# Kernel tuning notes

Measured on AMD Instinct MI355X. Metric: run time of the kernel, lower is better.

Reference implementation:

```python
import jax, jax.numpy as jnp
import numpy as np


def setup_inputs() -> dict:
    key = jax.random.key(0)
    k1, k2, k3 = jax.random.split(key, 3)
    B, E, N, D = 32, 8192, 2048, 128
    messages = jax.random.normal(k1, (B, E, D), dtype=jnp.float32)
    tgt_indices = jax.random.randint(k2, (B, E), 0, N, dtype=jnp.int32)
    atom_features_ref = jax.random.normal(k3, (B, N, D), dtype=jnp.float32)
    return {"messages": messages, "tgt_indices": tgt_indices,
            "atom_features_ref": atom_features_ref}


def reference(messages, tgt_indices, atom_features_ref):
    # Scatter-add edge messages to target atoms per batch element.
    # Equivalent to tf.scatter_nd with (batch, atom) index pairs, expressed
    # as a single flat segment_sum over offset indices batch*N + tgt.
    B, E, D = messages.shape
    N = atom_features_ref.shape[1]
    flat_seg = (jnp.arange(B, dtype=tgt_indices.dtype)[:, None] * N
                + tgt_indices).reshape(-1)            # (B*E,)
    flat_msg = messages.reshape(B * E, D)             # (B*E, D)
    agg = jax.ops.segment_sum(flat_msg, flat_seg, num_segments=B * N)
    return agg.reshape(B, N, D)
```

## Files before the change

### kernel.cpp

```cpp
#include <hip/hip_runtime.h>

#define BB    32
#define EE    8192
#define NN    2048
#define DD    128
#define ACH   64
#define NCH   (NN / ACH)
#define NTHR  512
#define NWAVE (NTHR / 64)
#define APW   (ACH / NWAVE)

__global__ __launch_bounds__(NTHR, 8) void scatter_seg_kernel(
    const float* __restrict__ messages,
    const int*   __restrict__ tgt,
    float*       __restrict__ out)
{
    __shared__ unsigned short lst[EE];
    __shared__ int cnt[ACH];
    __shared__ int off[ACH];
    __shared__ int cur[ACH];

    const int bid = blockIdx.x;
    const int b   = bid / NCH;
    const int a0  = (bid % NCH) * ACH;
    const int tid = threadIdx.x;
    const int w   = tid >> 6;
    const int l   = tid & 63;
    const int h   = l >> 5;
    const int c   = l & 31;

    if (tid < ACH) cnt[tid] = 0;
    __syncthreads();

    const int4* idx4 = (const int4*)(tgt + b * EE);
    for (int q = tid; q < EE / 4; q += NTHR) {
        int4 v = idx4[q];
        unsigned d;
        d = (unsigned)(v.x - a0); if (d < (unsigned)ACH) atomicAdd(&cnt[d], 1);
        d = (unsigned)(v.y - a0); if (d < (unsigned)ACH) atomicAdd(&cnt[d], 1);
        d = (unsigned)(v.z - a0); if (d < (unsigned)ACH) atomicAdd(&cnt[d], 1);
        d = (unsigned)(v.w - a0); if (d < (unsigned)ACH) atomicAdd(&cnt[d], 1);
    }
    __syncthreads();

    if (tid < 64) {
        int cc = cnt[tid];
        int s  = cc;
        #pragma unroll
        for (int sh = 1; sh < 64; sh <<= 1) {
            int t = __shfl_up(s, sh, 64);
            if (tid >= sh) s += t;
        }
        off[tid] = s - cc;
        cur[tid] = s - cc;
    }
    __syncthreads();

    for (int q = tid; q < EE / 4; q += NTHR) {
        int4 v = idx4[q];
        const int e = q * 4;
        unsigned d;
        d = (unsigned)(v.x - a0); if (d < (unsigned)ACH) { int p = atomicAdd(&cur[d], 1); lst[p] = (unsigned short)(e + 0); }
        d = (unsigned)(v.y - a0); if (d < (unsigned)ACH) { int p = atomicAdd(&cur[d], 1); lst[p] = (unsigned short)(e + 1); }
        d = (unsigned)(v.z - a0); if (d < (unsigned)ACH) { int p = atomicAdd(&cur[d], 1); lst[p] = (unsigned short)(e + 2); }
        d = (unsigned)(v.w - a0); if (d < (unsigned)ACH) { int p = atomicAdd(&cur[d], 1); lst[p] = (unsigned short)(e + 3); }
    }
    __syncthreads();

    const float4* msg4    = (const float4*)messages;
    const size_t  rowbase = (size_t)b * EE;
    float4*       out4    = (float4*)out;

    #pragma unroll
    for (int k = 0; k < APW / 2; ++k) {
        const int d   = w * APW + 2 * k + h;
        const int beg = off[d];
        const int n   = cnt[d];
        float4 s = make_float4(0.f, 0.f, 0.f, 0.f);
        int j = 0;
        for (; j + 4 <= n; j += 4) {
            int e0 = lst[beg + j + 0], e1 = lst[beg + j + 1];
            int e2 = lst[beg + j + 2], e3 = lst[beg + j + 3];
            float4 v0 = msg4[(rowbase + e0) * (DD / 4) + c];
            float4 v1 = msg4[(rowbase + e1) * (DD / 4) + c];
            float4 v2 = msg4[(rowbase + e2) * (DD / 4) + c];
            float4 v3 = msg4[(rowbase + e3) * (DD / 4) + c];
            s.x += (v0.x + v1.x) + (v2.x + v3.x);
            s.y += (v0.y + v1.y) + (v2.y + v3.y);
            s.z += (v0.z + v1.z) + (v2.z + v3.z);
            s.w += (v0.w + v1.w) + (v2.w + v3.w);
        }
        for (; j < n; ++j) {
            int e = lst[beg + j];
            float4 v = msg4[(rowbase + e) * (DD / 4) + c];
            s.x += v.x; s.y += v.y; s.z += v.z; s.w += v.w;
        }
        out4[((size_t)b * NN + a0 + d) * (DD / 4) + c] = s;
    }
}

extern "C" void kernel_launch(void* const* d_in, const int* in_sizes, int n_in,
                              void* d_out, int out_size, void* d_ws, size_t ws_size,
                              hipStream_t stream) {
    const float* messages = (const float*)d_in[0];
    const int*   tgt      = (const int*)d_in[1];
    float* out = (float*)d_out;

    dim3 grid(BB * NCH);
    scatter_seg_kernel<<<grid, NTHR, 0, stream>>>(messages, tgt, out);
}
```

Baseline: 223.7 us.

## Replace counting-sort bucket lists with fixed-slot per-atom lists and overflow fallback

Drops the separate counting pass and prefix scan over the target indices. Each block now makes one pass, appending edge ids into fixed 32-entry per-atom slots in shared memory. Atoms with more than 32 edges fall back to a full linear scan of the index array. This removes one read of the indices and two block barriers, and shrinks shared memory, but overflow atoms become very slow; with an average of 4 edges per atom, overflow should be rare.

```diff
diff --git a/kernel.cpp b/kernel.cpp
--- a/kernel.cpp
+++ b/kernel.cpp
@@ -9,16 +9,15 @@
 #define NTHR  512
 #define NWAVE (NTHR / 64)
 #define APW   (ACH / NWAVE)
+#define SLOT  32
 
-__global__ __launch_bounds__(NTHR, 8) void scatter_seg_kernel(
+__global__ __launch_bounds__(NTHR, 8) void scatter_slot_kernel(
     const float* __restrict__ messages,
     const int*   __restrict__ tgt,
     float*       __restrict__ out)
 {
-    __shared__ unsigned short lst[EE];
-    __shared__ int cnt[ACH];
-    __shared__ int off[ACH];
-    __shared__ int cur[ACH];
+    __shared__ unsigned short lst[ACH][SLOT];
+    __shared__ int            cnt[ACH];
 
     const int bid = blockIdx.x;
     const int b   = bid / NCH;
@@ -35,35 +34,12 @@
     const int4* idx4 = (const int4*)(tgt + b * EE);
     for (int q = tid; q < EE / 4; q += NTHR) {
         int4 v = idx4[q];
-        unsigned d;
-        d = (unsigned)(v.x - a0); if (d < (unsigned)ACH) atomicAdd(&cnt[d], 1);
-        d = (unsigned)(v.y - a0); if (d < (unsigned)ACH) atomicAdd(&cnt[d], 1);
-        d = (unsigned)(v.z - a0); if (d < (unsigned)ACH) atomicAdd(&cnt[d], 1);
-        d = (unsigned)(v.w - a0); if (d < (unsigned)ACH) atomicAdd(&cnt[d], 1);
-    }
-    __syncthreads();
-
-    if (tid < 64) {
-        int cc = cnt[tid];
-        int s  = cc;
-        #pragma unroll
-        for (int sh = 1; sh < 64; sh <<= 1) {
-            int t = __shfl_up(s, sh, 64);
-            if (tid >= sh) s += t;
-        }
-        off[tid] = s - cc;
-        cur[tid] = s - cc;
-    }
-    __syncthreads();
-
-    for (int q = tid; q < EE / 4; q += NTHR) {
-        int4 v = idx4[q];
         const int e = q * 4;
         unsigned d;
-        d = (unsigned)(v.x - a0); if (d < (unsigned)ACH) { int p = atomicAdd(&cur[d], 1); lst[p] = (unsigned short)(e + 0); }
-        d = (unsigned)(v.y - a0); if (d < (unsigned)ACH) { int p = atomicAdd(&cur[d], 1); lst[p] = (unsigned short)(e + 1); }
-        d = (unsigned)(v.z - a0); if (d < (unsigned)ACH) { int p = atomicAdd(&cur[d], 1); lst[p] = (unsigned short)(e + 2); }
-        d = (unsigned)(v.w - a0); if (d < (unsigned)ACH) { int p = atomicAdd(&cur[d], 1); lst[p] = (unsigned short)(e + 3); }
+        d = (unsigned)(v.x - a0); if (d < (unsigned)ACH) { int p = atomicAdd(&cnt[d], 1); if (p < SLOT) lst[d][p] = (unsigned short)(e + 0); }
+        d = (unsigned)(v.y - a0); if (d < (unsigned)ACH) { int p = atomicAdd(&cnt[d], 1); if (p < SLOT) lst[d][p] = (unsigned short)(e + 1); }
+        d = (unsigned)(v.z - a0); if (d < (unsigned)ACH) { int p = atomicAdd(&cnt[d], 1); if (p < SLOT) lst[d][p] = (unsigned short)(e + 2); }
+        d = (unsigned)(v.w - a0); if (d < (unsigned)ACH) { int p = atomicAdd(&cnt[d], 1); if (p < SLOT) lst[d][p] = (unsigned short)(e + 3); }
     }
     __syncthreads();
 
@@ -73,27 +49,37 @@
 
     #pragma unroll
     for (int k = 0; k < APW / 2; ++k) {
-        const int d   = w * APW + 2 * k + h;
-        const int beg = off[d];
-        const int n   = cnt[d];
+        const int d = w * APW + 2 * k + h;
+        const int n = cnt[d];
         float4 s = make_float4(0.f, 0.f, 0.f, 0.f);
-        int j = 0;
-        for (; j + 4 <= n; j += 4) {
-            int e0 = lst[beg + j + 0], e1 = lst[beg + j + 1];
-            int e2 = lst[beg + j + 2], e3 = lst[beg + j + 3];
-            float4 v0 = msg4[(rowbase + e0) * (DD / 4) + c];
-            float4 v1 = msg4[(rowbase + e1) * (DD / 4) + c];
-            float4 v2 = msg4[(rowbase + e2) * (DD / 4) + c];
-            float4 v3 = msg4[(rowbase + e3) * (DD / 4) + c];
-            s.x += (v0.x + v1.x) + (v2.x + v3.x);
-            s.y += (v0.y + v1.y) + (v2.y + v3.y);
-            s.z += (v0.z + v1.z) + (v2.z + v3.z);
-            s.w += (v0.w + v1.w) + (v2.w + v3.w);
-        }
-        for (; j < n; ++j) {
-            int e = lst[beg + j];
-            float4 v = msg4[(rowbase + e) * (DD / 4) + c];
-            s.x += v.x; s.y += v.y; s.z += v.z; s.w += v.w;
+        if (n <= SLOT) {
+            int j = 0;
+            for (; j + 4 <= n; j += 4) {
+                int e0 = lst[d][j + 0], e1 = lst[d][j + 1];
+                int e2 = lst[d][j + 2], e3 = lst[d][j + 3];
+                float4 v0 = msg4[(rowbase + e0) * (DD / 4) + c];
+                float4 v1 = msg4[(rowbase + e1) * (DD / 4) + c];
+                float4 v2 = msg4[(rowbase + e2) * (DD / 4) + c];
+                float4 v3 = msg4[(rowbase + e3) * (DD / 4) + c];
+                s.x += (v0.x + v1.x) + (v2.x + v3.x);
+                s.y += (v0.y + v1.y) + (v2.y + v3.y);
+                s.z += (v0.z + v1.z) + (v2.z + v3.z);
+                s.w += (v0.w + v1.w) + (v2.w + v3.w);
+            }
+            for (; j < n; ++j) {
+                int e = lst[d][j];
+                float4 v = msg4[(rowbase + e) * (DD / 4) + c];
+                s.x += v.x; s.y += v.y; s.z += v.z; s.w += v.w;
+            }
+        } else {
+            const int* idx = tgt + b * EE;
+            const int target = a0 + d;
+            for (int e = 0; e < EE; ++e) {
+                if (idx[e] == target) {
+                    float4 v = msg4[(rowbase + e) * (DD / 4) + c];
+                    s.x += v.x; s.y += v.y; s.z += v.z; s.w += v.w;
+                }
+            }
         }
         out4[((size_t)b * NN + a0 + d) * (DD / 4) + c] = s;
     }
@@ -107,5 +93,5 @@
     float* out = (float*)d_out;
 
     dim3 grid(BB * NCH);
-    scatter_seg_kernel<<<grid, NTHR, 0, stream>>>(messages, tgt, out);
+    scatter_slot_kernel<<<grid, NTHR, 0, stream>>>(messages, tgt, out);
 }
```

New measurement: 221.4 us. Within noise of the previous version (-1.1%).
